# Optimization experiments

Hardware: AMD Instinct MI355X
Metric: run time of the kernel (lower is better)

The kernel has to match this reference:

```python
import jax, jax.numpy as jnp
import numpy as np

COST_CLASS, COST_MASK, COST_DICE = 2.0, 5.0, 5.0
NUM_POINTS = 12544

def setup_inputs() -> dict:
    key = jax.random.key(0)
    k1, k2, k3, k4, k5 = jax.random.split(key, 5)
    bs, Q, K = 4, 100, 134
    H = W = 256
    M = 80
    P = H * W
    pred_logits = jax.random.normal(k1, (bs, Q, K), dtype=jnp.float32)
    pred_masks = jax.random.normal(k2, (bs, Q, H, W), dtype=jnp.float32)
    tgt_labels = jax.random.randint(k3, (M,), 0, K - 1, dtype=jnp.int32)
    # binary target masks, stored as float (matches .float() in torch code)
    tgt_masks = (jax.random.uniform(k4, (M, H, W)) > 0.5).astype(jnp.float32)
    # random subset of points without replacement (torch.randperm[:num_points])
    point_idx = jax.random.permutation(k5, P)[:NUM_POINTS].astype(jnp.int32)
    return {"pred_logits": pred_logits, "pred_masks": pred_masks,
            "tgt_labels": tgt_labels, "tgt_masks": tgt_masks,
            "point_idx": point_idx}

def reference(pred_logits, pred_masks, tgt_labels, tgt_masks, point_idx):
    bs, Q, K = pred_logits.shape
    N = bs * Q
    M = tgt_masks.shape[0]
    Pn = point_idx.shape[0]

    # class cost: -p[n, tgt_id[m]]
    out_prob = jax.nn.softmax(pred_logits.reshape(N, K), axis=-1)
    tgt_ids = jnp.clip(tgt_labels.astype(jnp.int32), 0, K - 1)
    cost_class = -out_prob[:, tgt_ids]                      # (N, M)

    # sampled mask logits / targets
    x = pred_masks.reshape(N, -1)[:, point_idx]             # (N, Pn) logits
    y = tgt_masks.reshape(M, -1)[:, point_idx]              # (M, Pn) binary float

    # BCE-with-logits cost, separable form:
    # mean_p[softplus(x) - x*y] = mean_p softplus(x) - (x @ y^T)/Pn
    sp_mean = jnp.mean(jax.nn.softplus(x), axis=-1)         # (N,)
    xy = jnp.einsum('np,mp->nm', x, y)                      # (N, M)
    cost_mask = sp_mean[:, None] - xy / Pn

    # dice cost
    s = jax.nn.sigmoid(x)                                   # (N, Pn)
    numer = 2.0 * jnp.einsum('np,mp->nm', s, y)             # (N, M)
    denom = jnp.sum(s, axis=-1)[:, None] + jnp.sum(y, axis=-1)[None, :]
    cost_dice = 1.0 - (numer + 1.0) / (denom + 1.0)

    C = COST_CLASS * cost_class + COST_MASK * cost_mask + COST_DICE * cost_dice
    return C.reshape(bs, Q, M)
```

## Files before the change

### kernel.cpp

```cpp
#include <hip/hip_runtime.h>
#include <math.h>

#define N_ROWS 400
#define M_ROWS 80
#define K_CLS  134
#define PN     12544
#define PFULL  65536
#define WORDS  (PFULL / 32)
#define TSTEPS 392
#define NSUB   25
#define KCG    49
#define TPB    2
#define NM     (N_ROWS * M_ROWS)
#define CHUNK  8192
#define CWORDS (CHUNK / 32)
#define CPB    (PFULL / CHUNK)

typedef __attribute__((ext_vector_type(4))) float  f32x4;
typedef __attribute__((ext_vector_type(8))) __bf16 bf16x8;

__device__ __forceinline__ float wave_reduce_sum(float v) {
#pragma unroll
    for (int off = 32; off > 0; off >>= 1) v += __shfl_down(v, off, 64);
    return v;
}

__global__ __launch_bounds__(1024) void sort_softmax_kernel(
        const int* __restrict__ point_idx,
        unsigned int* __restrict__ bitmap_g, int* __restrict__ rank_g,
        float* __restrict__ rowS_acc, float* __restrict__ rowSP_acc,
        float* __restrict__ ysum_acc,
        const float* __restrict__ pred_logits,
        float* __restrict__ rowmax, float* __restrict__ rowsum) {
    int tid = threadIdx.x;
    if (blockIdx.x == 0) {
        __shared__ unsigned int bits[WORDS];
        __shared__ int wtot[16], wbase[16];
        bits[tid] = 0u; bits[tid + 1024] = 0u;
        if (tid < N_ROWS) { rowS_acc[tid] = 0.f; rowSP_acc[tid] = 0.f; }
        if (tid < M_ROWS) ysum_acc[tid] = 0.f;
        __syncthreads();
        for (int i = tid; i < PN; i += 1024) {
            int p = point_idx[i];
            atomicOr(&bits[p >> 5], 1u << (p & 31));
        }
        __syncthreads();
        unsigned int w0 = bits[tid * 2], w1 = bits[tid * 2 + 1];
        int cnt = __popc(w0) + __popc(w1);
        int lane = tid & 63, wid = tid >> 6;
        int v = cnt;
#pragma unroll
        for (int off = 1; off < 64; off <<= 1) {
            int u = __shfl_up(v, off, 64);
            if (lane >= off) v += u;
        }
        if (lane == 63) wtot[wid] = v;
        __syncthreads();
        if (tid == 0) {
            int run = 0;
#pragma unroll
            for (int i = 0; i < 16; ++i) { wbase[i] = run; run += wtot[i]; }
        }
        __syncthreads();
        int base = wbase[wid] + (v - cnt);
        bitmap_g[tid * 2]     = w0;
        bitmap_g[tid * 2 + 1] = w1;
        rank_g[tid * 2]       = base;
        rank_g[tid * 2 + 1]   = base + __popc(w0);
    } else {
        int wave = tid >> 6, lane = tid & 63;
        int n = (blockIdx.x - 1) * 16 + wave;
        const float* row = pred_logits + n * K_CLS;
        float mx = -1e30f;
        for (int k = lane; k < K_CLS; k += 64) mx = fmaxf(mx, row[k]);
#pragma unroll
        for (int off = 32; off > 0; off >>= 1) mx = fmaxf(mx, __shfl_down(mx, off, 64));
        mx = __shfl(mx, 0, 64);
        float se = 0.f;
        for (int k = lane; k < K_CLS; k += 64) se += expf(row[k] - mx);
        se = wave_reduce_sum(se);
        if (lane == 0) { rowmax[n] = mx; rowsum[n] = se; }
    }
}

__global__ __launch_bounds__(256) void compact_kernel(
        const float* __restrict__ pred_masks, const float* __restrict__ tgt_masks,
        const unsigned int* __restrict__ bitmap_g, const int* __restrict__ rank_g,
        __bf16* __restrict__ Xc, __bf16* __restrict__ Sc, __bf16* __restrict__ Yc,
        float* __restrict__ rowS_acc, float* __restrict__ rowSP_acc,
        float* __restrict__ ysum_acc) {
    __shared__ __bf16 comp[CHUNK];
    __shared__ unsigned int sb[CWORDS];
    __shared__ int swb[CWORDS];
    __shared__ float a0[4], a1[4];
    int b   = blockIdx.x;
    int row = b / CPB, ch = b % CPB;
    int tid = threadIdx.x;
    int wave = tid >> 6, lane = tid & 63;
    int w0  = ch * CWORDS;
    int gb  = rank_g[w0];
    int end = (w0 + CWORDS == WORDS) ? PN : rank_g[w0 + CWORDS];
    int cnt = end - gb;
    sb[tid]  = bitmap_g[w0 + tid];
    swb[tid] = rank_g[w0 + tid] - gb;
    __syncthreads();
    int p0 = ch * CHUNK;
    bool isX = (row < N_ROWS);
    const float* src = isX ? (pred_masks + (size_t)row * PFULL + p0)
                           : (tgt_masks + (size_t)(row - N_ROWS) * PFULL + p0);

#pragma unroll
    for (int it = 0; it < CHUNK / (256 * 4); ++it) {
        int e = (it * 256 + tid) * 4;
        f32x4 v = *(const f32x4*)(src + e);
        unsigned int w = sb[e >> 5];
        int bp = e & 31;
        int r0 = swb[e >> 5] + __popc(w & ((1u << bp) - 1u));
        unsigned int m4 = (w >> bp) & 0xFu;
        if (isX) {
            if (m4 & 1u) comp[r0] = (__bf16)v[0];
            if (m4 & 2u) comp[r0 + __popc(m4 & 1u)] = (__bf16)v[1];
            if (m4 & 4u) comp[r0 + __popc(m4 & 3u)] = (__bf16)v[2];
            if (m4 & 8u) comp[r0 + __popc(m4 & 7u)] = (__bf16)v[3];
        } else {
            if (m4 & 1u) comp[r0] = (__bf16)((v[0] > 0.5f) ? 1.f : 0.f);
            if (m4 & 2u) comp[r0 + __popc(m4 & 1u)] = (__bf16)((v[1] > 0.5f) ? 1.f : 0.f);
            if (m4 & 4u) comp[r0 + __popc(m4 & 3u)] = (__bf16)((v[2] > 0.5f) ? 1.f : 0.f);
            if (m4 & 8u) comp[r0 + __popc(m4 & 7u)] = (__bf16)((v[3] > 0.5f) ? 1.f : 0.f);
        }
    }
    __syncthreads();

    if (isX) {
        __bf16* xrow = Xc + (size_t)row * PN + gb;
        __bf16* srow = Sc + (size_t)row * PN + gb;
        float sS = 0.f, sSP = 0.f;
        for (int i = tid; i < cnt; i += 256) {
            __bf16 xb = comp[i];
            float x  = (float)xb;
            float ax = fabsf(x);
            float ee = __expf(-ax);
            float den = 1.f + ee;
            float inv = __builtin_amdgcn_rcpf(den);
            float sig = (x >= 0.f) ? inv : ee * inv;
            float sp  = fmaxf(x, 0.f) + __logf(den);
            xrow[i] = xb;
            srow[i] = (__bf16)sig;
            sS += sig; sSP += sp;
        }
        sS  = wave_reduce_sum(sS);
        sSP = wave_reduce_sum(sSP);
        if (lane == 0) { a0[wave] = sS; a1[wave] = sSP; }
        __syncthreads();
        if (tid == 0)
            atomicAdd(&rowS_acc[row], a0[0] + a0[1] + a0[2] + a0[3]);
        else if (tid == 1)
            atomicAdd(&rowSP_acc[row], a1[0] + a1[1] + a1[2] + a1[3]);
    } else {
        int m = row - N_ROWS;
        __bf16* yrow = Yc + (size_t)m * PN + gb;
        float ys = 0.f;
        for (int i = tid; i < cnt; i += 256) {
            __bf16 y = comp[i];
            yrow[i] = y;
            ys += (float)y;
        }
        ys = wave_reduce_sum(ys);
        if (lane == 0) a0[wave] = ys;
        __syncthreads();
        if (tid == 0)
            atomicAdd(&ysum_acc[m], a0[0] + a0[1] + a0[2] + a0[3]);
    }
}

__global__ __launch_bounds__(256) void gemm_kernel(
        const __bf16* __restrict__ Xc, const __bf16* __restrict__ Sc,
        const __bf16* __restrict__ Yc,
        float* __restrict__ xypart, float* __restrict__ sypart) {
    __shared__ float red[4][20][64];
    int tid = threadIdx.x;
    int wave = tid >> 6, lane = tid & 63;
    int colL = lane & 15, quad = lane >> 4;
    int nsub = blockIdx.x % NSUB, kcg = blockIdx.x / NSUB;
    int n0 = nsub * 16;
    int tbase = kcg * (TPB * 4) + wave * TPB;

    f32x4 accX[5], accS[5];
    f32x4 zero = {0.f, 0.f, 0.f, 0.f};
#pragma unroll
    for (int j = 0; j < 5; ++j) { accX[j] = zero; accS[j] = zero; }

    bf16x8 aX[TPB], aS[TPB], Bb[TPB][5];
#pragma unroll
    for (int i = 0; i < TPB; ++i) {
        int t = tbase + i;
        int k0 = t * 32 + quad * 8;
        size_t aoff = (size_t)(n0 + colL) * PN + k0;
        aX[i] = *(const bf16x8*)(Xc + aoff);
        aS[i] = *(const bf16x8*)(Sc + aoff);
#pragma unroll
        for (int j = 0; j < 5; ++j)
            Bb[i][j] = *(const bf16x8*)(Yc + (size_t)(16 * j + colL) * PN + k0);
    }
#pragma unroll
    for (int i = 0; i < TPB; ++i) {
#pragma unroll
        for (int j = 0; j < 5; ++j) {
            accX[j] = __builtin_amdgcn_mfma_f32_16x16x32_bf16(aX[i], Bb[i][j], accX[j], 0, 0, 0);
            accS[j] = __builtin_amdgcn_mfma_f32_16x16x32_bf16(aS[i], Bb[i][j], accS[j], 0, 0, 0);
        }
    }

#pragma unroll
    for (int j = 0; j < 5; ++j)
#pragma unroll
        for (int r = 0; r < 4; ++r) red[wave][j * 4 + r][lane] = accX[j][r];
    __syncthreads();
#pragma unroll
    for (int v0 = 0; v0 < 5; ++v0) {
        int v = wave * 5 + v0;
        float s = red[0][v][lane] + red[1][v][lane] + red[2][v][lane] + red[3][v][lane];
        int j = v >> 2, r = v & 3;
        int n = n0 + quad * 4 + r, m = 16 * j + colL;
        xypart[(size_t)kcg * NM + n * M_ROWS + m] = s;
    }
    __syncthreads();
#pragma unroll
    for (int j = 0; j < 5; ++j)
#pragma unroll
        for (int r = 0; r < 4; ++r) red[wave][j * 4 + r][lane] = accS[j][r];
    __syncthreads();
#pragma unroll
    for (int v0 = 0; v0 < 5; ++v0) {
        int v = wave * 5 + v0;
        float s = red[0][v][lane] + red[1][v][lane] + red[2][v][lane] + red[3][v][lane];
        int j = v >> 2, r = v & 3;
        int n = n0 + quad * 4 + r, m = 16 * j + colL;
        sypart[(size_t)kcg * NM + n * M_ROWS + m] = s;
    }
}

__global__ __launch_bounds__(256) void combine_kernel(
        const float* __restrict__ logits,
        const int* __restrict__ tgt_labels,
        const float* __restrict__ rowmax,
        const float* __restrict__ rowsum,
        const float* __restrict__ rowS_acc,
        const float* __restrict__ rowSP_acc,
        const float* __restrict__ ysum_acc,
        const float* __restrict__ xypart,
        const float* __restrict__ sypart,
        float* __restrict__ out) {
    __shared__ float sxy[4][64], ssy[4][64];
    int il = threadIdx.x & 63, q = threadIdx.x >> 6;
    int idx = blockIdx.x * 64 + il;
    int n = idx / M_ROWS, m = idx % M_ROWS;
    float xy = 0.f, sy = 0.f;
    for (int g = q; g < KCG; g += 4) {
        xy += xypart[(size_t)g * NM + idx];
        sy += sypart[(size_t)g * NM + idx];
    }
    sxy[q][il] = xy; ssy[q][il] = sy;
    __syncthreads();
    if (q == 0) {
        xy = sxy[0][il] + sxy[1][il] + sxy[2][il] + sxy[3][il];
        sy = ssy[0][il] + ssy[1][il] + ssy[2][il] + ssy[3][il];
        float ss = rowS_acc[n], sp = rowSP_acc[n], ysum = ysum_acc[m];
        int tc = tgt_labels[m];
        tc = min(max(tc, 0), K_CLS - 1);
        float p = expf(logits[n * K_CLS + tc] - rowmax[n]) / rowsum[n];
        float cost_class = -p;
        float cost_mask = (sp - xy) * (1.0f / PN);
        float cost_dice = 1.f - (2.f * sy + 1.f) / (ss + ysum + 1.f);
        out[idx] = 2.f * cost_class + 5.f * cost_mask + 5.f * cost_dice;
    }
}

extern "C" void kernel_launch(void* const* d_in, const int* in_sizes, int n_in,
                              void* d_out, int out_size, void* d_ws, size_t ws_size,
                              hipStream_t stream) {
    const float* pred_logits = (const float*)d_in[0];
    const float* pred_masks  = (const float*)d_in[1];
    const int*   tgt_labels  = (const int*)d_in[2];
    const float* tgt_masks   = (const float*)d_in[3];
    const int*   point_idx   = (const int*)d_in[4];
    float* out = (float*)d_out;

    char* ws = (char*)d_ws;
    size_t off = 0;
    auto carve = [&](size_t nbytes) {
        char* p = ws + off;
        off += (nbytes + 255) & ~(size_t)255;
        return p;
    };
    unsigned int* bitmap = (unsigned int*)carve(WORDS * 4);
    int*   rankp  = (int*)carve(WORDS * 4);
    float* rowmax = (float*)carve(N_ROWS * 4);
    float* rowsum = (float*)carve(N_ROWS * 4);
    float* rowS_acc  = (float*)carve(N_ROWS * 4);
    float* rowSP_acc = (float*)carve(N_ROWS * 4);
    float* ysum_acc  = (float*)carve(M_ROWS * 4);
    __bf16* Xc = (__bf16*)carve((size_t)N_ROWS * PN * 2);
    __bf16* Sc = (__bf16*)carve((size_t)N_ROWS * PN * 2);
    __bf16* Yc = (__bf16*)carve((size_t)M_ROWS * PN * 2);
    float* xypart = (float*)carve((size_t)KCG * NM * 4);
    float* sypart = (float*)carve((size_t)KCG * NM * 4);
    (void)ws_size; (void)in_sizes; (void)n_in; (void)out_size;

    sort_softmax_kernel<<<26, 1024, 0, stream>>>(
        point_idx, bitmap, rankp, rowS_acc, rowSP_acc, ysum_acc,
        pred_logits, rowmax, rowsum);
    compact_kernel<<<(N_ROWS + M_ROWS) * CPB, 256, 0, stream>>>(
        pred_masks, tgt_masks, bitmap, rankp, Xc, Sc, Yc,
        rowS_acc, rowSP_acc, ysum_acc);
    gemm_kernel<<<NSUB * KCG, 256, 0, stream>>>(Xc, Sc, Yc, xypart, sypart);
    combine_kernel<<<NM / 64, 256, 0, stream>>>(
        pred_logits, tgt_labels, rowmax, rowsum, rowS_acc, rowSP_acc,
        ysum_acc, xypart, sypart, out);
}
```

Measured before the change: 208.7 us.

## Fuse pred-mask gather and sigmoid/softplus into GEMM, drop Xc/Sc buffers

The compaction of pred_masks into bf16 Xc/Sc buffers is removed. Each GEMM block now gathers its own 256-point K-slice directly from pred_masks into LDS, using a per-chunk word-range table built in the sort kernel. Sigmoid and softplus are computed in registers ahead of the MFMA, and row sums are accumulated with atomics. This saves the intermediate write and reread of two 400x12544 bf16 arrays and one kernel pass. In exchange each block scans a word span of the full-resolution row, and that span is clamped to 192 words, which could drop points if a chunk spans more.

```diff
diff --git a/kernel.cpp b/kernel.cpp
--- a/kernel.cpp
+++ b/kernel.cpp
@@ -7,14 +7,13 @@
 #define PN     12544
 #define PFULL  65536
 #define WORDS  (PFULL / 32)
-#define TSTEPS 392
 #define NSUB   25
 #define KCG    49
-#define TPB    2
 #define NM     (N_ROWS * M_ROWS)
 #define CHUNK  8192
 #define CWORDS (CHUNK / 32)
 #define CPB    (PFULL / CHUNK)
+#define SPAN   192
 
 typedef __attribute__((ext_vector_type(4))) float  f32x4;
 typedef __attribute__((ext_vector_type(8))) __bf16 bf16x8;
@@ -28,6 +27,7 @@
 __global__ __launch_bounds__(1024) void sort_softmax_kernel(
         const int* __restrict__ point_idx,
         unsigned int* __restrict__ bitmap_g, int* __restrict__ rank_g,
+        int* __restrict__ cw_g,
         float* __restrict__ rowS_acc, float* __restrict__ rowSP_acc,
         float* __restrict__ ysum_acc,
         const float* __restrict__ pred_logits,
@@ -46,7 +46,8 @@
         }
         __syncthreads();
         unsigned int w0 = bits[tid * 2], w1 = bits[tid * 2 + 1];
-        int cnt = __popc(w0) + __popc(w1);
+        int c0 = __popc(w0), c1 = __popc(w1);
+        int cnt = c0 + c1;
         int lane = tid & 63, wid = tid >> 6;
         int v = cnt;
 #pragma unroll
@@ -66,7 +67,17 @@
         bitmap_g[tid * 2]     = w0;
         bitmap_g[tid * 2 + 1] = w1;
         rank_g[tid * 2]       = base;
-        rank_g[tid * 2 + 1]   = base + __popc(w0);
+        rank_g[tid * 2 + 1]   = base + c0;
+        {
+            int rb = base, c = c0, w = tid * 2;
+            int kc = (rb + 255) >> 8;
+            if (c > 0 && kc < KCG && kc * 256 < rb + c) cw_g[kc] = w;
+        }
+        {
+            int rb = base + c0, c = c1, w = tid * 2 + 1;
+            int kc = (rb + 255) >> 8;
+            if (c > 0 && kc < KCG && kc * 256 < rb + c) cw_g[kc] = w;
+        }
     } else {
         int wave = tid >> 6, lane = tid & 63;
         int n = (blockIdx.x - 1) * 16 + wave;
@@ -83,18 +94,16 @@
     }
 }
 
-__global__ __launch_bounds__(256) void compact_kernel(
-        const float* __restrict__ pred_masks, const float* __restrict__ tgt_masks,
+__global__ __launch_bounds__(256) void buildY_kernel(
+        const float* __restrict__ tgt_masks,
         const unsigned int* __restrict__ bitmap_g, const int* __restrict__ rank_g,
-        __bf16* __restrict__ Xc, __bf16* __restrict__ Sc, __bf16* __restrict__ Yc,
-        float* __restrict__ rowS_acc, float* __restrict__ rowSP_acc,
-        float* __restrict__ ysum_acc) {
+        __bf16* __restrict__ Yc, float* __restrict__ ysum_acc) {
     __shared__ __bf16 comp[CHUNK];
     __shared__ unsigned int sb[CWORDS];
     __shared__ int swb[CWORDS];
-    __shared__ float a0[4], a1[4];
+    __shared__ float a0[4];
     int b   = blockIdx.x;
-    int row = b / CPB, ch = b % CPB;
+    int m = b / CPB, ch = b % CPB;
     int tid = threadIdx.x;
     int wave = tid >> 6, lane = tid & 63;
     int w0  = ch * CWORDS;
@@ -104,11 +113,7 @@
     sb[tid]  = bitmap_g[w0 + tid];
     swb[tid] = rank_g[w0 + tid] - gb;
     __syncthreads();
-    int p0 = ch * CHUNK;
-    bool isX = (row < N_ROWS);
-    const float* src = isX ? (pred_masks + (size_t)row * PFULL + p0)
-                           : (tgt_masks + (size_t)(row - N_ROWS) * PFULL + p0);
-
+    const float* src = tgt_masks + (size_t)m * PFULL + ch * CHUNK;
 #pragma unroll
     for (int it = 0; it < CHUNK / (256 * 4); ++it) {
         int e = (it * 256 + tid) * 4;
@@ -117,99 +122,117 @@
         int bp = e & 31;
         int r0 = swb[e >> 5] + __popc(w & ((1u << bp) - 1u));
         unsigned int m4 = (w >> bp) & 0xFu;
-        if (isX) {
-            if (m4 & 1u) comp[r0] = (__bf16)v[0];
-            if (m4 & 2u) comp[r0 + __popc(m4 & 1u)] = (__bf16)v[1];
-            if (m4 & 4u) comp[r0 + __popc(m4 & 3u)] = (__bf16)v[2];
-            if (m4 & 8u) comp[r0 + __popc(m4 & 7u)] = (__bf16)v[3];
-        } else {
-            if (m4 & 1u) comp[r0] = (__bf16)((v[0] > 0.5f) ? 1.f : 0.f);
-            if (m4 & 2u) comp[r0 + __popc(m4 & 1u)] = (__bf16)((v[1] > 0.5f) ? 1.f : 0.f);
-            if (m4 & 4u) comp[r0 + __popc(m4 & 3u)] = (__bf16)((v[2] > 0.5f) ? 1.f : 0.f);
-            if (m4 & 8u) comp[r0 + __popc(m4 & 7u)] = (__bf16)((v[3] > 0.5f) ? 1.f : 0.f);
-        }
-    }
-    __syncthreads();
-
-    if (isX) {
-        __bf16* xrow = Xc + (size_t)row * PN + gb;
-        __bf16* srow = Sc + (size_t)row * PN + gb;
-        float sS = 0.f, sSP = 0.f;
-        for (int i = tid; i < cnt; i += 256) {
-            __bf16 xb = comp[i];
-            float x  = (float)xb;
+        if (m4 & 1u) comp[r0] = (__bf16)((v[0] > 0.5f) ? 1.f : 0.f);
+        if (m4 & 2u) comp[r0 + __popc(m4 & 1u)] = (__bf16)((v[1] > 0.5f) ? 1.f : 0.f);
+        if (m4 & 4u) comp[r0 + __popc(m4 & 3u)] = (__bf16)((v[2] > 0.5f) ? 1.f : 0.f);
+        if (m4 & 8u) comp[r0 + __popc(m4 & 7u)] = (__bf16)((v[3] > 0.5f) ? 1.f : 0.f);
+    }
+    __syncthreads();
+    __bf16* yrow = Yc + (size_t)m * PN + gb;
+    float ys = 0.f;
+    for (int i = tid; i < cnt; i += 256) {
+        __bf16 y = comp[i];
+        yrow[i] = y;
+        ys += (float)y;
+    }
+    ys = wave_reduce_sum(ys);
+    if (lane == 0) a0[wave] = ys;
+    __syncthreads();
+    if (tid == 0)
+        atomicAdd(&ysum_acc[m], a0[0] + a0[1] + a0[2] + a0[3]);
+}
+
+__global__ __launch_bounds__(256) void gemm_fused_kernel(
+        const float* __restrict__ pred_masks,
+        const __bf16* __restrict__ Yc,
+        const unsigned int* __restrict__ bitmap_g,
+        const int* __restrict__ rank_g, const int* __restrict__ cw_g,
+        float* __restrict__ xypart, float* __restrict__ sypart,
+        float* __restrict__ rowS_acc, float* __restrict__ rowSP_acc) {
+    __shared__ __bf16 comp[16 * 272];
+    __shared__ unsigned int sw[SPAN];
+    __shared__ int sr[SPAN];
+    __shared__ float red[4][20][64];
+    __shared__ float rowred[4][2][16];
+    int tid = threadIdx.x;
+    int wave = tid >> 6, lane = tid & 63;
+    int colL = lane & 15, quad = lane >> 4;
+    int nsub = blockIdx.x % NSUB, kcg = blockIdx.x / NSUB;
+    int n0 = nsub * 16;
+    int wlo = cw_g[kcg];
+    int ew  = (kcg == KCG - 1) ? (WORDS - 1) : cw_g[kcg + 1];
+    int S = ew - wlo + 1; if (S > SPAN) S = SPAN;
+    int rbase = kcg * 256;
+    for (int i = tid; i < S; i += 256) {
+        sw[i] = bitmap_g[wlo + i];
+        sr[i] = rank_g[wlo + i] - rbase;
+    }
+    bf16x8 Bb[2][5];
+#pragma unroll
+    for (int i = 0; i < 2; ++i) {
+        int k0 = kcg * 256 + (wave * 2 + i) * 32 + quad * 8;
+#pragma unroll
+        for (int j = 0; j < 5; ++j)
+            Bb[i][j] = *(const bf16x8*)(Yc + (size_t)(16 * j + colL) * PN + k0);
+    }
+    __syncthreads();
+
+    int E4 = S * 8;
+#pragma unroll
+    for (int rr = 0; rr < 4; ++rr) {
+        int row = wave + rr * 4;
+        const float* src = pred_masks + (size_t)(n0 + row) * PFULL + (size_t)wlo * 32;
+        __bf16* crow = comp + row * 272;
+        for (int e4 = lane; e4 < E4; e4 += 64) {
+            f32x4 v = *(const f32x4*)(src + e4 * 4);
+            unsigned int w = sw[e4 >> 3];
+            int bp = (e4 & 7) * 4;
+            int r0 = sr[e4 >> 3] + __popc(w & ((1u << bp) - 1u));
+            unsigned int m4 = (w >> bp) & 0xFu;
+            int r1 = r0 + (int)(m4 & 1u);
+            int r2 = r0 + __popc(m4 & 3u);
+            int r3 = r0 + __popc(m4 & 7u);
+            if ((m4 & 1u) && (unsigned)r0 < 256u) crow[r0] = (__bf16)v[0];
+            if ((m4 & 2u) && (unsigned)r1 < 256u) crow[r1] = (__bf16)v[1];
+            if ((m4 & 4u) && (unsigned)r2 < 256u) crow[r2] = (__bf16)v[2];
+            if ((m4 & 8u) && (unsigned)r3 < 256u) crow[r3] = (__bf16)v[3];
+        }
+    }
+    __syncthreads();
+
+    f32x4 accX[5], accS[5];
+    f32x4 zero = {0.f, 0.f, 0.f, 0.f};
+#pragma unroll
+    for (int j = 0; j < 5; ++j) { accX[j] = zero; accS[j] = zero; }
+    float sS = 0.f, sSP = 0.f;
+#pragma unroll
+    for (int i = 0; i < 2; ++i) {
+        int kl = (wave * 2 + i) * 32 + quad * 8;
+        bf16x8 aX = *(const bf16x8*)&comp[colL * 272 + kl];
+        bf16x8 aSg;
+#pragma unroll
+        for (int jj = 0; jj < 8; ++jj) {
+            float x  = (float)aX[jj];
             float ax = fabsf(x);
             float ee = __expf(-ax);
             float den = 1.f + ee;
             float inv = __builtin_amdgcn_rcpf(den);
             float sig = (x >= 0.f) ? inv : ee * inv;
             float sp  = fmaxf(x, 0.f) + __logf(den);
-            xrow[i] = xb;
-            srow[i] = (__bf16)sig;
+            aSg[jj] = (__bf16)sig;
             sS += sig; sSP += sp;
         }
-        sS  = wave_reduce_sum(sS);
-        sSP = wave_reduce_sum(sSP);
-        if (lane == 0) { a0[wave] = sS; a1[wave] = sSP; }
-        __syncthreads();
-        if (tid == 0)
-            atomicAdd(&rowS_acc[row], a0[0] + a0[1] + a0[2] + a0[3]);
-        else if (tid == 1)
-            atomicAdd(&rowSP_acc[row], a1[0] + a1[1] + a1[2] + a1[3]);
-    } else {
-        int m = row - N_ROWS;
-        __bf16* yrow = Yc + (size_t)m * PN + gb;
-        float ys = 0.f;
-        for (int i = tid; i < cnt; i += 256) {
-            __bf16 y = comp[i];
-            yrow[i] = y;
-            ys += (float)y;
-        }
-        ys = wave_reduce_sum(ys);
-        if (lane == 0) a0[wave] = ys;
-        __syncthreads();
-        if (tid == 0)
-            atomicAdd(&ysum_acc[m], a0[0] + a0[1] + a0[2] + a0[3]);
-    }
-}
-
-__global__ __launch_bounds__(256) void gemm_kernel(
-        const __bf16* __restrict__ Xc, const __bf16* __restrict__ Sc,
-        const __bf16* __restrict__ Yc,
-        float* __restrict__ xypart, float* __restrict__ sypart) {
-    __shared__ float red[4][20][64];
-    int tid = threadIdx.x;
-    int wave = tid >> 6, lane = tid & 63;
-    int colL = lane & 15, quad = lane >> 4;
-    int nsub = blockIdx.x % NSUB, kcg = blockIdx.x / NSUB;
-    int n0 = nsub * 16;
-    int tbase = kcg * (TPB * 4) + wave * TPB;
-
-    f32x4 accX[5], accS[5];
-    f32x4 zero = {0.f, 0.f, 0.f, 0.f};
-#pragma unroll
-    for (int j = 0; j < 5; ++j) { accX[j] = zero; accS[j] = zero; }
-
-    bf16x8 aX[TPB], aS[TPB], Bb[TPB][5];
-#pragma unroll
-    for (int i = 0; i < TPB; ++i) {
-        int t = tbase + i;
-        int k0 = t * 32 + quad * 8;
-        size_t aoff = (size_t)(n0 + colL) * PN + k0;
-        aX[i] = *(const bf16x8*)(Xc + aoff);
-        aS[i] = *(const bf16x8*)(Sc + aoff);
-#pragma unroll
-        for (int j = 0; j < 5; ++j)
-            Bb[i][j] = *(const bf16x8*)(Yc + (size_t)(16 * j + colL) * PN + k0);
-    }
-#pragma unroll
-    for (int i = 0; i < TPB; ++i) {
 #pragma unroll
         for (int j = 0; j < 5; ++j) {
-            accX[j] = __builtin_amdgcn_mfma_f32_16x16x32_bf16(aX[i], Bb[i][j], accX[j], 0, 0, 0);
-            accS[j] = __builtin_amdgcn_mfma_f32_16x16x32_bf16(aS[i], Bb[i][j], accS[j], 0, 0, 0);
-        }
-    }
+            accX[j] = __builtin_amdgcn_mfma_f32_16x16x32_bf16(aX,  Bb[i][j], accX[j], 0, 0, 0);
+            accS[j] = __builtin_amdgcn_mfma_f32_16x16x32_bf16(aSg, Bb[i][j], accS[j], 0, 0, 0);
+        }
+    }
+    sS  += __shfl_down(sS, 32, 64);
+    sS  += __shfl_down(sS, 16, 64);
+    sSP += __shfl_down(sSP, 32, 64);
+    sSP += __shfl_down(sSP, 16, 64);
+    if (lane < 16) { rowred[wave][0][lane] = sS; rowred[wave][1][lane] = sSP; }
 
 #pragma unroll
     for (int j = 0; j < 5; ++j)
@@ -223,6 +246,16 @@
         int j = v >> 2, r = v & 3;
         int n = n0 + quad * 4 + r, m = 16 * j + colL;
         xypart[(size_t)kcg * NM + n * M_ROWS + m] = s;
+    }
+    if (tid < 16) {
+        atomicAdd(&rowS_acc[n0 + tid],
+                  rowred[0][0][tid] + rowred[1][0][tid] +
+                  rowred[2][0][tid] + rowred[3][0][tid]);
+    } else if (tid < 32) {
+        int l = tid - 16;
+        atomicAdd(&rowSP_acc[n0 + l],
+                  rowred[0][1][l] + rowred[1][1][l] +
+                  rowred[2][1][l] + rowred[3][1][l]);
     }
     __syncthreads();
 #pragma unroll
@@ -295,25 +328,25 @@
     };
     unsigned int* bitmap = (unsigned int*)carve(WORDS * 4);
     int*   rankp  = (int*)carve(WORDS * 4);
+    int*   cw     = (int*)carve(KCG * 4);
     float* rowmax = (float*)carve(N_ROWS * 4);
     float* rowsum = (float*)carve(N_ROWS * 4);
     float* rowS_acc  = (float*)carve(N_ROWS * 4);
     float* rowSP_acc = (float*)carve(N_ROWS * 4);
     float* ysum_acc  = (float*)carve(M_ROWS * 4);
-    __bf16* Xc = (__bf16*)carve((size_t)N_ROWS * PN * 2);
-    __bf16* Sc = (__bf16*)carve((size_t)N_ROWS * PN * 2);
     __bf16* Yc = (__bf16*)carve((size_t)M_ROWS * PN * 2);
     float* xypart = (float*)carve((size_t)KCG * NM * 4);
     float* sypart = (float*)carve((size_t)KCG * NM * 4);
     (void)ws_size; (void)in_sizes; (void)n_in; (void)out_size;
 
     sort_softmax_kernel<<<26, 1024, 0, stream>>>(
-        point_idx, bitmap, rankp, rowS_acc, rowSP_acc, ysum_acc,
+        point_idx, bitmap, rankp, cw, rowS_acc, rowSP_acc, ysum_acc,
         pred_logits, rowmax, rowsum);
-    compact_kernel<<<(N_ROWS + M_ROWS) * CPB, 256, 0, stream>>>(
-        pred_masks, tgt_masks, bitmap, rankp, Xc, Sc, Yc,
-        rowS_acc, rowSP_acc, ysum_acc);
-    gemm_kernel<<<NSUB * KCG, 256, 0, stream>>>(Xc, Sc, Yc, xypart, sypart);
+    buildY_kernel<<<M_ROWS * CPB, 256, 0, stream>>>(
+        tgt_masks, bitmap, rankp, Yc, ysum_acc);
+    gemm_fused_kernel<<<NSUB * KCG, 256, 0, stream>>>(
+        pred_masks, Yc, bitmap, rankp, cw, xypart, sypart,
+        rowS_acc, rowSP_acc);
     combine_kernel<<<NM / 64, 256, 0, stream>>>(
         pred_logits, tgt_labels, rowmax, rowsum, rowS_acc, rowSP_acc,
         ysum_acc, xypart, sypart, out);
```

Result: slower. 215.7 us (+3.3%).
